# Kernel optimization log

Measured on AMD Instinct MI355X. Metric: run time of the kernel, lower is better.

Reference implementation:

```python
import jax, jax.numpy as jnp
import numpy as np

N_HEAD = 16
N_KV_HEAD = 4
HEAD_DIM = 64  # n_embd // n_head = 1024 // 16
N_EMBD = 1024


def _alibi_bias(T, n_head, head_dim):
    # slopes: start = 2**(-2**(-(log2(H)-3))); slope_i = start**(i+1)
    start = 2.0 ** (-2.0 ** (-(np.log2(n_head) - 3.0)))
    slopes = jnp.asarray(start ** np.arange(1, n_head + 1), dtype=jnp.float32)  # [H]
    rel = (jnp.arange(T, dtype=jnp.float32)[None, :]
           - jnp.arange(T, dtype=jnp.float32)[:, None])  # [T,T], rel[i,j] = j - i
    bias = slopes[:, None, None] * rel[None, :, :]  # [H,T,T]
    # Faithful to the torch module: masked_fill(-inf) is then OVERWRITTEN by
    # torch.tril, which zeroes the upper triangle. Net effect: lower-tri alibi
    # values, 0 above the diagonal (NO causal masking).
    bias = jnp.tril(bias)
    return bias * (head_dim ** -0.5)  # extra scale applied in forward


def setup_inputs() -> dict:
    key = jax.random.key(0)
    ks = jax.random.split(key, 5)
    B, T, C = 4, 2048, N_EMBD
    w_scale = 0.02
    return {
        "x": jax.random.normal(ks[0], (B, T, C), dtype=jnp.float32),
        "Wq": jax.random.normal(ks[1], (C, C), dtype=jnp.float32) * w_scale,
        "Wkv": jax.random.normal(ks[2], (2 * N_KV_HEAD * HEAD_DIM, C), dtype=jnp.float32) * w_scale,
        "Wproj": jax.random.normal(ks[3], (C, C), dtype=jnp.float32) * w_scale,
        "bproj": jnp.zeros((C,), dtype=jnp.float32),
    }


def reference(x, Wq, Wkv, Wproj, bproj):
    B, T, C = x.shape
    H, KVH, D = N_HEAD, N_KV_HEAD, HEAD_DIM
    ratio = H // KVH

    q = jnp.einsum('btc,ec->bte', x, Wq).reshape(B, T, H, D).transpose(0, 2, 1, 3)  # [B,H,T,D]
    kv = jnp.einsum('btc,ec->bte', x, Wkv)  # [B,T,2*KVH*D]
    k, v = jnp.split(kv, 2, axis=-1)
    k = k.reshape(B, T, KVH, D).transpose(0, 2, 1, 3)  # [B,KVH,T,D]
    v = v.reshape(B, T, KVH, D).transpose(0, 2, 1, 3)
    # torch .repeat tiles whole blocks: query head h uses kv head h % KVH
    k = jnp.tile(k, (1, ratio, 1, 1))  # [B,H,T,D]
    v = jnp.tile(v, (1, ratio, 1, 1))

    bias = _alibi_bias(T, H, D)  # [H,T,T], already *= D**-0.5
    scores = jnp.einsum('bhtd,bhsd->bhts', q, k) * (D ** -0.5) + bias[None]
    attn = jax.nn.softmax(scores, axis=-1)
    out = jnp.einsum('bhts,bhsd->bhtd', attn, v)  # [B,H,T,D]
    out = out.transpose(0, 2, 1, 3).reshape(B, T, C)
    return jnp.einsum('btc,ec->bte', out, Wproj) + bproj
```

## Files before the change

kernel.cpp:

```cpp
#include <hip/hip_runtime.h>
#include <hip/hip_bf16.h>
#include <cstdint>

typedef __bf16 bf16;
typedef bf16 bf16x2 __attribute__((ext_vector_type(2)));
typedef bf16 bf16x4 __attribute__((ext_vector_type(4)));
typedef bf16 bf16x8 __attribute__((ext_vector_type(8)));
typedef _Float16 f16;
typedef f16 f16x2 __attribute__((ext_vector_type(2)));
typedef f16 f16x4 __attribute__((ext_vector_type(4)));
typedef f16 f16x8 __attribute__((ext_vector_type(8)));
typedef float f32x4 __attribute__((ext_vector_type(4)));

#define MFMA16(a, b, c) __builtin_amdgcn_mfma_f32_16x16x32_bf16((a), (b), (c), 0, 0, 0)
#define MFMA16H(a, b, c) __builtin_amdgcn_mfma_f32_16x16x16f16((a), (b), (c), 0, 0, 0)

#define QSCALE 0.18033688011112042f

__device__ inline void async16(const bf16* g, bf16* l) {
  __builtin_amdgcn_global_load_lds(
      (const __attribute__((address_space(1))) void*)g,
      (__attribute__((address_space(3))) void*)l, 16, 0, 0);
}

__global__ void cast_all(const float* __restrict__ x, const float* __restrict__ wq,
                         const float* __restrict__ wkv, const float* __restrict__ wp,
                         bf16* __restrict__ xb, bf16* __restrict__ w1b,
                         bf16* __restrict__ wpb) {
  const int i = blockIdx.x * blockDim.x + threadIdx.x;
  const float4* src;
  bf16x4* dst;
  int idx;
  if (i < 2097152) {
    src = (const float4*)x; dst = (bf16x4*)xb; idx = i;
  } else if (i < 2359296) {
    src = (const float4*)wq; dst = (bf16x4*)w1b; idx = i - 2097152;
  } else if (i < 2490368) {
    src = (const float4*)wkv; dst = (bf16x4*)(w1b + 1048576); idx = i - 2359296;
  } else {
    src = (const float4*)wp; dst = (bf16x4*)wpb; idx = i - 2490368;
  }
  const float4 v = src[idx];
  bf16x4 o;
  o.x = (bf16)v.x; o.y = (bf16)v.y; o.z = (bf16)v.z; o.w = (bf16)v.w;
  dst[idx] = o;
}

__global__ __launch_bounds__(256, 2)
void gemm_qkv(const bf16* __restrict__ A, const bf16* __restrict__ B,
              bf16* __restrict__ qb, bf16* __restrict__ kb, f16* __restrict__ vb) {
  constexpr int K = 1024;
  __shared__ bf16 sA[128 * 64];
  __shared__ bf16 sB[128 * 64];
  const int tid = threadIdx.x;
  const int lane = tid & 63, wid = tid >> 6;
  const int col = lane & 15, quad = lane >> 4;
  const int wm = wid >> 1, wn = wid & 1;
  const int m0 = blockIdx.y * 128, n0 = blockIdx.x * 128;
  const int c7 = col & 7;

  f32x4 acc[4][4];
  const f32x4 z = {0.f, 0.f, 0.f, 0.f};
#pragma unroll
  for (int mi = 0; mi < 4; mi++)
#pragma unroll
    for (int ni = 0; ni < 4; ni++) acc[mi][ni] = z;

  for (int k0 = 0; k0 < K; k0 += 64) {
    __syncthreads();
#pragma unroll
    for (int c = 0; c < 4; ++c) {
      const int idx = c * 256 + tid;
      const int row = idx >> 3, kc = idx & 7;
      const int gkc = kc ^ (row & 7);
      async16(&A[(size_t)(m0 + row) * K + k0 + gkc * 8], &sA[idx * 8]);
      async16(&B[(size_t)(n0 + row) * K + k0 + gkc * 8], &sB[idx * 8]);
    }
    __syncthreads();
#pragma unroll
    for (int ks = 0; ks < 2; ++ks) {
      bf16x8 af[4], bfr[4];
#pragma unroll
      for (int i = 0; i < 4; i++)
        af[i] = *(const bf16x8*)&sA[(wm * 64 + i * 16 + col) * 64 +
                                    (((ks * 4 + quad) ^ c7) << 3)];
#pragma unroll
      for (int i = 0; i < 4; i++)
        bfr[i] = *(const bf16x8*)&sB[(wn * 64 + i * 16 + col) * 64 +
                                     (((ks * 4 + quad) ^ c7) << 3)];
#pragma unroll
      for (int mi = 0; mi < 4; mi++)
#pragma unroll
        for (int ni = 0; ni < 4; ni++)
          acc[mi][ni] = MFMA16(af[mi], bfr[ni], acc[mi][ni]);
    }
  }
#pragma unroll
  for (int mi = 0; mi < 4; mi++) {
#pragma unroll
    for (int ni = 0; ni < 4; ni++) {
      const int e = n0 + wn * 64 + ni * 16 + col;
#pragma unroll
      for (int r = 0; r < 4; r++) {
        const int m = m0 + wm * 64 + mi * 16 + quad * 4 + r;
        const int bb = m >> 11, t = m & 2047;
        if (e < 1024) {
          qb[(((size_t)bb * 16 + (e >> 6)) * 2048 + t) * 64 + (e & 63)] =
              (bf16)(acc[mi][ni][r] * QSCALE);
        } else if (e < 1280) {
          const int f = e - 1024;
          kb[(((size_t)bb * 4 + (f >> 6)) * 2048 + t) * 64 + (f & 63)] =
              (bf16)acc[mi][ni][r];
        } else {
          const int f = e - 1280;
          vb[(((size_t)bb * 4 + (f >> 6)) * 2048 + t) * 64 + (f & 63)] =
              (f16)acc[mi][ni][r];
        }
      }
    }
  }
}

__global__ __launch_bounds__(256, 2)
void gemm_proj(const bf16* __restrict__ A, const bf16* __restrict__ B,
               const float* __restrict__ bias, float* __restrict__ out) {
  constexpr int K = 1024;
  __shared__ bf16 sA[128 * 64];
  __shared__ bf16 sB[128 * 64];
  const int tid = threadIdx.x;
  const int lane = tid & 63, wid = tid >> 6;
  const int col = lane & 15, quad = lane >> 4;
  const int wm = wid >> 1, wn = wid & 1;
  const int m0 = blockIdx.y * 128, n0 = blockIdx.x * 128;
  const int c7 = col & 7;

  f32x4 acc[4][4];
  const f32x4 z = {0.f, 0.f, 0.f, 0.f};
#pragma unroll
  for (int mi = 0; mi < 4; mi++)
#pragma unroll
    for (int ni = 0; ni < 4; ni++) acc[mi][ni] = z;

  for (int k0 = 0; k0 < K; k0 += 64) {
    __syncthreads();
#pragma unroll
    for (int c = 0; c < 4; ++c) {
      const int idx = c * 256 + tid;
      const int row = idx >> 3, kc = idx & 7;
      const int gkc = kc ^ (row & 7);
      async16(&A[(size_t)(m0 + row) * K + k0 + gkc * 8], &sA[idx * 8]);
      async16(&B[(size_t)(n0 + row) * K + k0 + gkc * 8], &sB[idx * 8]);
    }
    __syncthreads();
#pragma unroll
    for (int ks = 0; ks < 2; ++ks) {
      bf16x8 af[4], bfr[4];
#pragma unroll
      for (int i = 0; i < 4; i++)
        af[i] = *(const bf16x8*)&sA[(wm * 64 + i * 16 + col) * 64 +
                                    (((ks * 4 + quad) ^ c7) << 3)];
#pragma unroll
      for (int i = 0; i < 4; i++)
        bfr[i] = *(const bf16x8*)&sB[(wn * 64 + i * 16 + col) * 64 +
                                     (((ks * 4 + quad) ^ c7) << 3)];
#pragma unroll
      for (int mi = 0; mi < 4; mi++)
#pragma unroll
        for (int ni = 0; ni < 4; ni++)
          acc[mi][ni] = MFMA16(af[mi], bfr[ni], acc[mi][ni]);
    }
  }
#pragma unroll
  for (int mi = 0; mi < 4; mi++) {
#pragma unroll
    for (int ni = 0; ni < 4; ni++) {
      const int e = n0 + wn * 64 + ni * 16 + col;
      const float be = bias[e];
#pragma unroll
      for (int r = 0; r < 4; r++) {
        const int m = m0 + wm * 64 + mi * 16 + quad * 4 + r;
        out[(size_t)m * 1024 + e] = acc[mi][ni][r] + be;
      }
    }
  }
}

__global__ __launch_bounds__(256, 2)
void attn_alibi(const bf16* __restrict__ qb, const bf16* __restrict__ kbp,
                const f16* __restrict__ vbp, bf16* __restrict__ ob) {
  __shared__ f16 sVt[2][64 * 72];
  const int tid = threadIdx.x;
  const int lane = tid & 63, wid = tid >> 6;
  const int col = lane & 15, quad = lane >> 4;
  const int bh = blockIdx.y;
  const int b = bh >> 4, h = bh & 15, kvh = h & 3;
  const int qbase = __builtin_amdgcn_readfirstlane(blockIdx.x * 256 + wid * 64);

  const bf16* qptr = qb + ((size_t)(b * 16 + h) * 2048 + qbase) * 64;
  const bf16* kptr = kbp + ((size_t)(b * 4 + kvh) * 2048) * 64;
  const f16* vptr = vbp + ((size_t)(b * 4 + kvh) * 2048) * 64;

  bf16x8 bq[4][2];
#pragma unroll
  for (int ni = 0; ni < 4; ni++)
#pragma unroll
    for (int ks = 0; ks < 2; ks++)
      bq[ni][ks] = *(const bf16x8*)&qptr[(ni * 16 + col) * 64 + ks * 32 + quad * 8];

  f16x4 ones;
#pragma unroll
  for (int j = 0; j < 4; j++) ones[j] = (f16)1.0f;

  f32x4 OT[4][4];
  f32x4 lC[4];
  const f32x4 z = {0.f, 0.f, 0.f, 0.f};
#pragma unroll
  for (int nd = 0; nd < 4; nd++) {
    lC[nd] = z;
#pragma unroll
    for (int ni = 0; ni < 4; ni++) OT[nd][ni] = z;
  }

  const float cb = exp2f(-0.5f * (float)(h + 1)) * QSCALE;
  const int qoff = quad * 4 - col;

  bf16x8 ak[4][2];
#pragma unroll
  for (int mi = 0; mi < 4; mi++)
#pragma unroll
    for (int ks = 0; ks < 2; ks++)
      ak[mi][ks] = *(const bf16x8*)&kptr[(size_t)(mi * 16 + col) * 64 + ks * 32 + quad * 8];

  const int pv = tid & 31, kcv = tid >> 5;
  f16x8 vr0 = *(const f16x8*)&vptr[(size_t)(2 * pv) * 64 + kcv * 8];
  f16x8 vr1 = *(const f16x8*)&vptr[(size_t)(2 * pv + 1) * 64 + kcv * 8];

  int bufi = 0;
  for (int c0 = 0; c0 < 2048; c0 += 64, bufi ^= 1) {
    f16* sv = sVt[bufi];
#pragma unroll
    for (int j = 0; j < 8; j++) {
      f16x2 pr;
      pr.x = vr0[j];
      pr.y = vr1[j];
      *(f16x2*)&sv[(kcv * 8 + j) * 72 + 2 * pv] = pr;
    }
    __syncthreads();

    const int cn = (c0 + 64 < 2048) ? c0 + 64 : 0;
    bf16x8 akn[4][2];
#pragma unroll
    for (int mi = 0; mi < 4; mi++)
#pragma unroll
      for (int ks = 0; ks < 2; ks++)
        akn[mi][ks] = *(const bf16x8*)&kptr[(size_t)(cn + mi * 16 + col) * 64 +
                                            ks * 32 + quad * 8];
    f16x8 vr0n = *(const f16x8*)&vptr[(size_t)(cn + 2 * pv) * 64 + kcv * 8];
    f16x8 vr1n = *(const f16x8*)&vptr[(size_t)(cn + 2 * pv + 1) * 64 + kcv * 8];

    f32x4 S[4][4];
#pragma unroll
    for (int kb = 0; kb < 4; kb++)
#pragma unroll
      for (int ni = 0; ni < 4; ni++) S[kb][ni] = z;
#pragma unroll
    for (int ks = 0; ks < 2; ks++)
#pragma unroll
      for (int kb = 0; kb < 4; kb++)
#pragma unroll
        for (int ni = 0; ni < 4; ni++)
          S[kb][ni] = MFMA16(ak[kb][ks], bq[ni][ks], S[kb][ni]);

#pragma unroll
    for (int kb = 0; kb < 4; kb++) {
      f16x4 pf[4];
#pragma unroll
      for (int ni = 0; ni < 4; ni++) {
        const int U = c0 + kb * 16 - qbase - ni * 16;
        f32x4 p;
        if (U <= -15) {
          const float bb = cb * (float)(U + qoff);
#pragma unroll
          for (int r = 0; r < 4; r++)
            p[r] = __builtin_amdgcn_exp2f(S[kb][ni][r] + (bb + cb * (float)r));
        } else if (U >= 16) {
#pragma unroll
          for (int r = 0; r < 4; r++)
            p[r] = __builtin_amdgcn_exp2f(S[kb][ni][r]);
        } else {
          const float relf = (float)(U + qoff);
#pragma unroll
          for (int r = 0; r < 4; r++) {
            const float rr = relf + (float)r;
            const float bb = (rr <= 0.f) ? cb * rr : 0.f;
            p[r] = __builtin_amdgcn_exp2f(S[kb][ni][r] + bb);
          }
        }
#pragma unroll
        for (int r = 0; r < 4; r++) pf[ni][r] = (f16)p[r];
      }
      f16x4 av[4];
#pragma unroll
      for (int nd = 0; nd < 4; nd++)
        av[nd] = *(const f16x4*)&sv[(nd * 16 + col) * 72 + kb * 16 + quad * 4];
#pragma unroll
      for (int ni = 0; ni < 4; ni++) {
#pragma unroll
        for (int nd = 0; nd < 4; nd++)
          OT[nd][ni] = MFMA16H(av[nd], pf[ni], OT[nd][ni]);
        lC[ni] = MFMA16H(ones, pf[ni], lC[ni]);
      }
    }

#pragma unroll
    for (int mi = 0; mi < 4; mi++)
#pragma unroll
      for (int ks = 0; ks < 2; ks++) ak[mi][ks] = akn[mi][ks];
    vr0 = vr0n;
    vr1 = vr1n;
  }

#pragma unroll
  for (int ni = 0; ni < 4; ni++) {
    const float inv = 1.0f / lC[ni][0];
    const size_t rowb = ((size_t)b * 2048 + qbase + ni * 16 + col) * 1024 + h * 64;
#pragma unroll
    for (int nd = 0; nd < 4; nd++) {
      bf16x4 w;
#pragma unroll
      for (int r = 0; r < 4; r++) w[r] = (bf16)(OT[nd][ni][r] * inv);
      *(bf16x4*)&ob[rowb + nd * 16 + quad * 4] = w;
    }
  }
}

extern "C" void kernel_launch(void* const* d_in, const int* in_sizes, int n_in,
                              void* d_out, int out_size, void* d_ws, size_t ws_size,
                              hipStream_t stream) {
  const float* x     = (const float*)d_in[0];
  const float* Wq    = (const float*)d_in[1];
  const float* Wkv   = (const float*)d_in[2];
  const float* Wproj = (const float*)d_in[3];
  const float* bproj = (const float*)d_in[4];
  float* out = (float*)d_out;

  bf16* xb  = (bf16*)d_ws;
  bf16* w1b = xb  + 8388608;
  bf16* wpb = w1b + 1572864;
  bf16* qb  = wpb + 1048576;
  bf16* kb  = qb  + 8388608;
  f16*  vb  = (f16*)(kb + 2097152);
  bf16* aob = (bf16*)(vb + 2097152);

  cast_all<<<10752, 256, 0, stream>>>(x, Wq, Wkv, Wproj, xb, w1b, wpb);
  gemm_qkv<<<dim3(12, 64), 256, 0, stream>>>(xb, w1b, qb, kb, vb);
  attn_alibi<<<dim3(8, 64), 256, 0, stream>>>(qb, kb, vb, aob);
  gemm_proj<<<dim3(8, 64), 256, 0, stream>>>(aob, wpb, bproj, out);
}
```

Measured before the change: 259.2 us.

## Split attention KV range across two blocks, stage K/P in LDS, add combine kernel

The attention kernel now splits the 2048-key range into two halves along a new grid z dimension, which doubles the number of blocks. It writes unnormalized fp16 partial outputs plus per-row sums, and a new combine kernel normalizes them to bf16. K is staged through swizzled LDS instead of per-lane register loads. P is written to LDS so the PV product can use the wider 16x16x32 f16 MFMA, and the row sum is accumulated with scalar adds instead of a ones-MFMA. This raises occupancy and parallelism, at the cost of extra partial-output traffic, one more kernel launch, and added LDS round trips. No running max is used, so the two unnormalized halves can be summed directly.

Result: slower. 634.4 us (+144.8%).

```diff
diff --git a/kernel.cpp b/kernel.cpp
--- a/kernel.cpp
+++ b/kernel.cpp
@@ -3,7 +3,6 @@
 #include <cstdint>
 
 typedef __bf16 bf16;
-typedef bf16 bf16x2 __attribute__((ext_vector_type(2)));
 typedef bf16 bf16x4 __attribute__((ext_vector_type(4)));
 typedef bf16 bf16x8 __attribute__((ext_vector_type(8)));
 typedef _Float16 f16;
@@ -13,7 +12,7 @@
 typedef float f32x4 __attribute__((ext_vector_type(4)));
 
 #define MFMA16(a, b, c) __builtin_amdgcn_mfma_f32_16x16x32_bf16((a), (b), (c), 0, 0, 0)
-#define MFMA16H(a, b, c) __builtin_amdgcn_mfma_f32_16x16x16f16((a), (b), (c), 0, 0, 0)
+#define MFMA16HF(a, b, c) __builtin_amdgcn_mfma_f32_16x16x32_f16((a), (b), (c), 0, 0, 0)
 
 #define QSCALE 0.18033688011112042f
 
@@ -185,20 +184,26 @@
   }
 }
 
-__global__ __launch_bounds__(256, 2)
+__global__ __launch_bounds__(256, 3)
 void attn_alibi(const bf16* __restrict__ qb, const bf16* __restrict__ kbp,
-                const f16* __restrict__ vbp, bf16* __restrict__ ob) {
-  __shared__ f16 sVt[2][64 * 72];
+                const f16* __restrict__ vbp, f16* __restrict__ op0,
+                f16* __restrict__ op1, float* __restrict__ lpart) {
+  __shared__ bf16 sK[64 * 64];
+  __shared__ f16 sVt[64 * 72];
+  __shared__ f16 sPh[4][64 * 32];
   const int tid = threadIdx.x;
   const int lane = tid & 63, wid = tid >> 6;
   const int col = lane & 15, quad = lane >> 4;
+  const int c7 = col & 7;
   const int bh = blockIdx.y;
   const int b = bh >> 4, h = bh & 15, kvh = h & 3;
   const int qbase = __builtin_amdgcn_readfirstlane(blockIdx.x * 256 + wid * 64);
+  const int zb = blockIdx.z;
+  const int kvbase = zb * 1024;
 
   const bf16* qptr = qb + ((size_t)(b * 16 + h) * 2048 + qbase) * 64;
-  const bf16* kptr = kbp + ((size_t)(b * 4 + kvh) * 2048) * 64;
-  const f16* vptr = vbp + ((size_t)(b * 4 + kvh) * 2048) * 64;
+  const bf16* kptr = kbp + ((size_t)((b * 4 + kvh) * 2048 + kvbase)) * 64;
+  const f16* vptr = vbp + ((size_t)((b * 4 + kvh) * 2048 + kvbase)) * 64;
 
   bf16x8 bq[4][2];
 #pragma unroll
@@ -207,131 +212,161 @@
     for (int ks = 0; ks < 2; ks++)
       bq[ni][ks] = *(const bf16x8*)&qptr[(ni * 16 + col) * 64 + ks * 32 + quad * 8];
 
-  f16x4 ones;
-#pragma unroll
-  for (int j = 0; j < 4; j++) ones[j] = (f16)1.0f;
-
   f32x4 OT[4][4];
-  f32x4 lC[4];
+  float lsum[4] = {0.f, 0.f, 0.f, 0.f};
   const f32x4 z = {0.f, 0.f, 0.f, 0.f};
 #pragma unroll
-  for (int nd = 0; nd < 4; nd++) {
-    lC[nd] = z;
+  for (int nd = 0; nd < 4; nd++)
 #pragma unroll
     for (int ni = 0; ni < 4; ni++) OT[nd][ni] = z;
-  }
 
   const float cb = exp2f(-0.5f * (float)(h + 1)) * QSCALE;
   const int qoff = quad * 4 - col;
 
-  bf16x8 ak[4][2];
-#pragma unroll
-  for (int mi = 0; mi < 4; mi++)
-#pragma unroll
-    for (int ks = 0; ks < 2; ks++)
-      ak[mi][ks] = *(const bf16x8*)&kptr[(size_t)(mi * 16 + col) * 64 + ks * 32 + quad * 8];
-
-  const int pv = tid & 31, kcv = tid >> 5;
-  f16x8 vr0 = *(const f16x8*)&vptr[(size_t)(2 * pv) * 64 + kcv * 8];
-  f16x8 vr1 = *(const f16x8*)&vptr[(size_t)(2 * pv + 1) * 64 + kcv * 8];
-
-  int bufi = 0;
-  for (int c0 = 0; c0 < 2048; c0 += 64, bufi ^= 1) {
-    f16* sv = sVt[bufi];
+  const int rk0 = tid >> 3, rk1 = 32 + rk0, kc = tid & 7;
+  const int rv = rk0 * 2;
+  const int blkv = rv >> 3, rlv = rv & 7;
+  const int kx = (kc ^ (rk0 & 7)) << 3;
+
+  bf16x8 kr0 = *(const bf16x8*)&kptr[(size_t)rk0 * 64 + kc * 8];
+  bf16x8 kr1 = *(const bf16x8*)&kptr[(size_t)rk1 * 64 + kc * 8];
+  f16x8 vr0 = *(const f16x8*)&vptr[(size_t)rv * 64 + kc * 8];
+  f16x8 vr1 = *(const f16x8*)&vptr[(size_t)(rv + 1) * 64 + kc * 8];
+
+  f16* sp = sPh[wid];
+
+  for (int cc = 0; cc < 16; ++cc) {
+    const int c0 = kvbase + cc * 64;
+    __syncthreads();
+    *(bf16x8*)&sK[rk0 * 64 + kx] = kr0;
+    *(bf16x8*)&sK[rk1 * 64 + kx] = kr1;
 #pragma unroll
     for (int j = 0; j < 8; j++) {
       f16x2 pr;
       pr.x = vr0[j];
       pr.y = vr1[j];
-      *(f16x2*)&sv[(kcv * 8 + j) * 72 + 2 * pv] = pr;
-    }
-    __syncthreads();
-
-    const int cn = (c0 + 64 < 2048) ? c0 + 64 : 0;
-    bf16x8 akn[4][2];
-#pragma unroll
-    for (int mi = 0; mi < 4; mi++)
-#pragma unroll
-      for (int ks = 0; ks < 2; ks++)
-        akn[mi][ks] = *(const bf16x8*)&kptr[(size_t)(cn + mi * 16 + col) * 64 +
-                                            ks * 32 + quad * 8];
-    f16x8 vr0n = *(const f16x8*)&vptr[(size_t)(cn + 2 * pv) * 64 + kcv * 8];
-    f16x8 vr1n = *(const f16x8*)&vptr[(size_t)(cn + 2 * pv + 1) * 64 + kcv * 8];
-
-    f32x4 S[4][4];
-#pragma unroll
-    for (int kb = 0; kb < 4; kb++)
-#pragma unroll
-      for (int ni = 0; ni < 4; ni++) S[kb][ni] = z;
-#pragma unroll
-    for (int ks = 0; ks < 2; ks++)
-#pragma unroll
-      for (int kb = 0; kb < 4; kb++)
-#pragma unroll
-        for (int ni = 0; ni < 4; ni++)
-          S[kb][ni] = MFMA16(ak[kb][ks], bq[ni][ks], S[kb][ni]);
-
-#pragma unroll
-    for (int kb = 0; kb < 4; kb++) {
-      f16x4 pf[4];
+      *(f16x2*)&sVt[(kc * 8 + j) * 72 + ((blkv ^ kc) << 3) + rlv] = pr;
+    }
+    __syncthreads();
+
+    {
+      const int cof = (cc + 1 < 16) ? (cc + 1) * 64 : 0;
+      kr0 = *(const bf16x8*)&kptr[(size_t)(cof + rk0) * 64 + kc * 8];
+      kr1 = *(const bf16x8*)&kptr[(size_t)(cof + rk1) * 64 + kc * 8];
+      vr0 = *(const f16x8*)&vptr[(size_t)(cof + rv) * 64 + kc * 8];
+      vr1 = *(const f16x8*)&vptr[(size_t)(cof + rv + 1) * 64 + kc * 8];
+    }
+
+#pragma unroll
+    for (int half = 0; half < 2; half++) {
+#pragma unroll
+      for (int kb2 = 0; kb2 < 2; kb2++) {
+        const int kb = half * 2 + kb2;
+        bf16x8 ak[2];
+#pragma unroll
+        for (int ks = 0; ks < 2; ks++)
+          ak[ks] = *(const bf16x8*)&sK[(kb * 16 + col) * 64 +
+                                       (((ks * 4 + quad) ^ c7) << 3)];
+        f32x4 S[4];
+#pragma unroll
+        for (int ni = 0; ni < 4; ni++) S[ni] = z;
+#pragma unroll
+        for (int ks = 0; ks < 2; ks++)
+#pragma unroll
+          for (int ni = 0; ni < 4; ni++)
+            S[ni] = MFMA16(ak[ks], bq[ni][ks], S[ni]);
+
+#pragma unroll
+        for (int ni = 0; ni < 4; ni++) {
+          const int U = c0 + kb * 16 - qbase - ni * 16;
+          f32x4 p;
+          if (U <= -15) {
+            const float bb = cb * (float)(U + qoff);
+#pragma unroll
+            for (int r = 0; r < 4; r++)
+              p[r] = __builtin_amdgcn_exp2f(S[ni][r] + (bb + cb * (float)r));
+          } else if (U >= 16) {
+#pragma unroll
+            for (int r = 0; r < 4; r++)
+              p[r] = __builtin_amdgcn_exp2f(S[ni][r]);
+          } else {
+            const float relf = (float)(U + qoff);
+#pragma unroll
+            for (int r = 0; r < 4; r++) {
+              const float rr = relf + (float)r;
+              const float bb = (rr <= 0.f) ? cb * rr : 0.f;
+              p[r] = __builtin_amdgcn_exp2f(S[ni][r] + bb);
+            }
+          }
+          lsum[ni] += (p[0] + p[1]) + (p[2] + p[3]);
+          f16x4 w;
+#pragma unroll
+          for (int r = 0; r < 4; r++) w[r] = (f16)p[r];
+          *(f16x4*)&sp[((ni * 16 + col) << 5) + (((kb2 * 4 + quad) ^ c7) << 2)] = w;
+        }
+      }
+
+      f16x8 av[4], pb[4];
+#pragma unroll
+      for (int nd = 0; nd < 4; nd++) {
+        const int d = nd * 16 + col;
+        av[nd] = *(const f16x8*)&sVt[d * 72 + (((half * 4 + quad) ^ (d >> 3)) << 3)];
+      }
 #pragma unroll
       for (int ni = 0; ni < 4; ni++) {
-        const int U = c0 + kb * 16 - qbase - ni * 16;
-        f32x4 p;
-        if (U <= -15) {
-          const float bb = cb * (float)(U + qoff);
-#pragma unroll
-          for (int r = 0; r < 4; r++)
-            p[r] = __builtin_amdgcn_exp2f(S[kb][ni][r] + (bb + cb * (float)r));
-        } else if (U >= 16) {
-#pragma unroll
-          for (int r = 0; r < 4; r++)
-            p[r] = __builtin_amdgcn_exp2f(S[kb][ni][r]);
-        } else {
-          const float relf = (float)(U + qoff);
-#pragma unroll
-          for (int r = 0; r < 4; r++) {
-            const float rr = relf + (float)r;
-            const float bb = (rr <= 0.f) ? cb * rr : 0.f;
-            p[r] = __builtin_amdgcn_exp2f(S[kb][ni][r] + bb);
-          }
-        }
-#pragma unroll
-        for (int r = 0; r < 4; r++) pf[ni][r] = (f16)p[r];
-      }
-      f16x4 av[4];
-#pragma unroll
-      for (int nd = 0; nd < 4; nd++)
-        av[nd] = *(const f16x4*)&sv[(nd * 16 + col) * 72 + kb * 16 + quad * 4];
-#pragma unroll
-      for (int ni = 0; ni < 4; ni++) {
+        const int rowo = (ni * 16 + col) << 5;
+        *(f16x4*)&pb[ni] = *(const f16x4*)&sp[rowo + (((2 * quad) ^ c7) << 2)];
+        *((f16x4*)&pb[ni] + 1) = *(const f16x4*)&sp[rowo + (((2 * quad + 1) ^ c7) << 2)];
+      }
+#pragma unroll
+      for (int ni = 0; ni < 4; ni++)
 #pragma unroll
         for (int nd = 0; nd < 4; nd++)
-          OT[nd][ni] = MFMA16H(av[nd], pf[ni], OT[nd][ni]);
-        lC[ni] = MFMA16H(ones, pf[ni], lC[ni]);
-      }
-    }
-
-#pragma unroll
-    for (int mi = 0; mi < 4; mi++)
-#pragma unroll
-      for (int ks = 0; ks < 2; ks++) ak[mi][ks] = akn[mi][ks];
-    vr0 = vr0n;
-    vr1 = vr1n;
+          OT[nd][ni] = MFMA16HF(av[nd], pb[ni], OT[nd][ni]);
+    }
   }
 
 #pragma unroll
   for (int ni = 0; ni < 4; ni++) {
-    const float inv = 1.0f / lC[ni][0];
-    const size_t rowb = ((size_t)b * 2048 + qbase + ni * 16 + col) * 1024 + h * 64;
+    float l = lsum[ni];
+    l += __shfl_xor(l, 16);
+    l += __shfl_xor(l, 32);
+    lsum[ni] = l;
+  }
+
+  f16* op = zb ? op1 : op0;
+#pragma unroll
+  for (int ni = 0; ni < 4; ni++) {
+    const int t = qbase + ni * 16 + col;
+    const size_t rowb = ((size_t)b * 2048 + t) * 1024 + h * 64;
 #pragma unroll
     for (int nd = 0; nd < 4; nd++) {
-      bf16x4 w;
-#pragma unroll
-      for (int r = 0; r < 4; r++) w[r] = (bf16)(OT[nd][ni][r] * inv);
-      *(bf16x4*)&ob[rowb + nd * 16 + quad * 4] = w;
-    }
-  }
+      f16x4 w;
+#pragma unroll
+      for (int r = 0; r < 4; r++) w[r] = (f16)OT[nd][ni][r];
+      *(f16x4*)&op[rowb + nd * 16 + quad * 4] = w;
+    }
+    if (quad == 0)
+      lpart[zb * 131072 + (b * 16 + h) * 2048 + t] = lsum[ni];
+  }
+}
+
+__global__ void combine(const f16* __restrict__ op0, const f16* __restrict__ op1,
+                        const float* __restrict__ lpart, bf16* __restrict__ aob) {
+  const int i = blockIdx.x * 256 + threadIdx.x;
+  const size_t base = (size_t)i * 8;
+  const int row = (int)(base >> 10);
+  const int e = (int)(base & 1023);
+  const int b = row >> 11, t = row & 2047;
+  const int h = e >> 6;
+  const int li = (b * 16 + h) * 2048 + t;
+  const float inv = 1.0f / (lpart[li] + lpart[131072 + li]);
+  const f16x8 a = *(const f16x8*)&op0[base];
+  const f16x8 c = *(const f16x8*)&op1[base];
+  bf16x8 o;
+#pragma unroll
+  for (int j = 0; j < 8; j++) o[j] = (bf16)(((float)a[j] + (float)c[j]) * inv);
+  *(bf16x8*)&aob[base] = o;
 }
 
 extern "C" void kernel_launch(void* const* d_in, const int* in_sizes, int n_in,
@@ -344,16 +379,21 @@
   const float* bproj = (const float*)d_in[4];
   float* out = (float*)d_out;
 
-  bf16* xb  = (bf16*)d_ws;
-  bf16* w1b = xb  + 8388608;
-  bf16* wpb = w1b + 1572864;
-  bf16* qb  = wpb + 1048576;
-  bf16* kb  = qb  + 8388608;
-  f16*  vb  = (f16*)(kb + 2097152);
-  bf16* aob = (bf16*)(vb + 2097152);
+  bf16* xb   = (bf16*)d_ws;
+  bf16* w1b  = xb + 8388608;
+  bf16* wpb  = w1b + 1572864;
+  bf16* qb   = wpb + 1048576;
+  bf16* kb   = qb + 8388608;
+  f16*  vb   = (f16*)(kb + 2097152);
+  f16*  op1  = (f16*)(vb + 2097152);
+
+  f16*   op0   = (f16*)xb;
+  float* lpart = (float*)w1b;
+  bf16*  aob   = qb;
 
   cast_all<<<10752, 256, 0, stream>>>(x, Wq, Wkv, Wproj, xb, w1b, wpb);
   gemm_qkv<<<dim3(12, 64), 256, 0, stream>>>(xb, w1b, qb, kb, vb);
-  attn_alibi<<<dim3(8, 64), 256, 0, stream>>>(qb, kb, vb, aob);
+  attn_alibi<<<dim3(8, 64, 2), 256, 0, stream>>>(qb, kb, vb, op0, op1, lpart);
+  combine<<<4096, 256, 0, stream>>>(op0, op1, lpart, aob);
   gemm_proj<<<dim3(8, 64), 256, 0, stream>>>(aob, wpb, bproj, out);
 }
```
